# Performance work log

Measured on AMD Instinct MI355X. Metric: run time of the kernel, lower is better.

Reference implementation:

```python
import jax, jax.numpy as jnp
import numpy as np

D_MODEL = 1024
N_HEAD = 16
D_HEAD = 64
BN, T = 4, 2048


def setup_inputs() -> dict:
    key = jax.random.key(0)
    k1, k2, k3, k4 = jax.random.split(key, 4)
    x = jax.random.normal(k1, (BN, T, D_MODEL), dtype=jnp.float32)
    mask = jax.random.randint(k2, (BN, T), 0, 2, dtype=jnp.int32)
    # to_qkv: Linear(d_model, 3*d_cat, bias=False); torch weight shape [out, in]
    w_qkv = jax.random.normal(k3, (3 * N_HEAD * D_HEAD, D_MODEL), dtype=jnp.float32) / np.sqrt(D_MODEL)
    w_tail = jax.random.normal(k4, (D_MODEL, N_HEAD * D_HEAD), dtype=jnp.float32) / np.sqrt(N_HEAD * D_HEAD)
    b_tail = jnp.zeros((D_MODEL,), dtype=jnp.float32)
    return {"x": x, "mask": mask, "w_qkv": w_qkv, "w_tail": w_tail, "b_tail": b_tail}


def reference(x, mask, w_qkv, w_tail, b_tail):
    bn, t, _ = x.shape
    scale = D_HEAD ** -0.5
    # qkv: [bn, t, 3*h*d] -> view(bn,t,h,3*d) -> chunk(3) along last dim
    qkv = jnp.einsum('btm,om->bto', x, w_qkv)
    qkv = qkv.reshape(bn, t, N_HEAD, 3, D_HEAD)  # chunk layout: [q|k|v] per head
    q = qkv[..., 0, :].transpose(0, 2, 1, 3)  # [bn, h, t, d]
    k = qkv[..., 1, :].transpose(0, 2, 1, 3)
    v = qkv[..., 2, :].transpose(0, 2, 1, 3)
    dots = jnp.einsum('bhqd,bhkd->bhqk', q, k) * scale  # [bn, h, t, t]
    keep = (mask != 0)[:, None, None, :]  # [bn, 1, 1, t]
    dots = jnp.where(keep, dots, -jnp.inf)
    coef = jax.nn.softmax(dots, axis=-1)  # dropout p=0 -> identity
    attn = jnp.einsum('bhqk,bhkd->bhqd', coef, v)
    out = attn.transpose(0, 2, 1, 3).reshape(bn, t, N_HEAD * D_HEAD)
    out = jnp.einsum('btc,oc->bto', out, w_tail) + b_tail
    return out
```

## Files before the change

kernel.cpp:

```cpp
#include <hip/hip_runtime.h>
#include <hip/hip_bf16.h>
#include <stdint.h>


typedef __attribute__((ext_vector_type(8))) short short8;
typedef __attribute__((ext_vector_type(4))) short short4b;
typedef __attribute__((ext_vector_type(4))) float f32x4;

#define T_SEQ 2048
#define NHEAD 16
#define DHEAD 64
#define DMODEL 1024

#if __has_builtin(__builtin_amdgcn_exp2f)
#define EXP2(x) __builtin_amdgcn_exp2f(x)
#else
#define EXP2(x) exp2f(x)
#endif

__device__ __forceinline__ ushort f2bf(float f) {
  __bf16 h = (__bf16)f;
  unsigned short u;
  __builtin_memcpy(&u, &h, 2);
  return u;
}
__device__ __forceinline__ float bf2f(ushort b) {
  return __uint_as_float(((uint32_t)b) << 16);
}

__device__ __forceinline__ int permInv(int x) {
  return (x & 0x23) | ((x & 0x0C) << 1) | ((x & 0x10) >> 2);
}

__device__ __forceinline__ void gload_lds16(const ushort* g, ushort* l) {
  __builtin_amdgcn_global_load_lds(
      (const __attribute__((address_space(1))) void*)g,
      (__attribute__((address_space(3))) void*)l, 16, 0, 0);
}

__global__ void cvt_all(const float* __restrict__ x,
                        const float* __restrict__ wq,
                        const float* __restrict__ wt,
                        ushort* __restrict__ out,
                        int n8x, int n8q, int n8t) {
  int i = blockIdx.x * blockDim.x + threadIdx.x;
  const float* src;
  int j;
  if (i < n8x) { src = x; j = i; }
  else if (i < n8x + n8q) { src = wq; j = i - n8x; }
  else if (i < n8x + n8q + n8t) { src = wt; j = i - n8x - n8q; }
  else return;
  const float4* p = (const float4*)(src + (size_t)j * 8);
  float4 a = p[0], b = p[1];
  short8 o;
  o[0] = (short)f2bf(a.x); o[1] = (short)f2bf(a.y);
  o[2] = (short)f2bf(a.z); o[3] = (short)f2bf(a.w);
  o[4] = (short)f2bf(b.x); o[5] = (short)f2bf(b.y);
  o[6] = (short)f2bf(b.z); o[7] = (short)f2bf(b.w);
  *(short8*)(out + (size_t)i * 8) = o;
}

template <int EPI>
__launch_bounds__(256)
__global__ void gemm_bt(const ushort* __restrict__ A,
                        const ushort* __restrict__ B,
                        void* __restrict__ Cout,
                        const float* __restrict__ bias,
                        const int* __restrict__ msk,
                        int M, int N, int K) {
  __shared__ ushort sA[2][128 * 64];
  __shared__ ushort sB[2][128 * 64];
  const int tid = threadIdx.x;
  const int lane = tid & 63;
  const int wid = tid >> 6;
  const int wr = wid >> 1, wc = wid & 1;
  const int bm = blockIdx.x * 128;
  const int bn = blockIdx.y * 128;
  const int l15 = lane & 15;
  const int lg = lane >> 4;

  f32x4 acc[4][4] = {};

  auto STAGE = [&](int buf, int k0) {
#pragma unroll
    for (int r = 0; r < 4; ++r) {
      int c = r * 256 + tid;
      int row = c >> 3, ci = c & 7;
      gload_lds16(A + (size_t)(bm + row) * K + k0 + ci * 8, &sA[buf][c * 8]);
      gload_lds16(B + (size_t)(bn + row) * K + k0 + ci * 8, &sB[buf][c * 8]);
    }
  };

  STAGE(0, 0);
  __syncthreads();

  const int nk = K >> 6;
  for (int kt = 0; kt < nk; ++kt) {
    const int cur = kt & 1;
    if (kt + 1 < nk) STAGE(cur ^ 1, (kt + 1) << 6);
#pragma unroll
    for (int ks = 0; ks < 2; ++ks) {
      short8 af[4], bfr[4];
#pragma unroll
      for (int m = 0; m < 4; ++m)
        af[m] = *(const short8*)&sA[cur][(wr * 64 + m * 16 + l15) * 64 + ks * 32 + lg * 8];
#pragma unroll
      for (int n = 0; n < 4; ++n)
        bfr[n] = *(const short8*)&sB[cur][(wc * 64 + n * 16 + l15) * 64 + ks * 32 + lg * 8];
      __builtin_amdgcn_s_setprio(1);
#pragma unroll
      for (int m = 0; m < 4; ++m)
#pragma unroll
        for (int n = 0; n < 4; ++n)
          acc[m][n] = __builtin_amdgcn_mfma_f32_16x16x32_bf16(af[m], bfr[n], acc[m][n], 0, 0, 0);
      __builtin_amdgcn_s_setprio(0);
    }
    __syncthreads();
  }

  if (EPI == 0) {
    ushort* qkvb = (ushort*)Cout;
    const int b = bm >> 11;
    int mk[4][4];
#pragma unroll
    for (int m = 0; m < 4; ++m)
#pragma unroll
      for (int r = 0; r < 4; ++r) {
        int gr = bm + wr * 64 + m * 16 + lg * 4 + r;
        mk[m][r] = msk[b * T_SEQ + (gr & (T_SEQ - 1))];
      }
#pragma unroll
    for (int m = 0; m < 4; ++m)
#pragma unroll
      for (int n = 0; n < 4; ++n)
#pragma unroll
        for (int r = 0; r < 4; ++r) {
          int gr = bm + wr * 64 + m * 16 + lg * 4 + r;
          int gc = bn + wc * 64 + n * 16 + l15;
          int t = gr & (T_SEQ - 1);
          int h = gc / 192, rem = gc - h * 192;
          int sel = rem >> 6, d = rem & 63;
          size_t base = (size_t)((b * NHEAD + h) * 3 + sel) * T_SEQ * DHEAD;
          float v = acc[m][n][r];
          size_t dst;
          if (sel == 2) {
            int tp = (t & ~63) | permInv(t & 63);
            if (!mk[m][r]) v = 0.f;
            dst = base + (size_t)d * T_SEQ + tp;
          } else {
            dst = base + (size_t)t * DHEAD + d;
          }
          qkvb[dst] = f2bf(v);
        }
  } else {
    float* out = (float*)Cout;
#pragma unroll
    for (int m = 0; m < 4; ++m)
#pragma unroll
      for (int n = 0; n < 4; ++n) {
        int gc = bn + wc * 64 + n * 16 + l15;
        float bv = bias[gc];
#pragma unroll
        for (int r = 0; r < 4; ++r) {
          int gr = bm + wr * 64 + m * 16 + lg * 4 + r;
          out[(size_t)gr * N + gc] = acc[m][n][r] + bv;
        }
      }
  }
}

__launch_bounds__(256)
__global__ void attn_fwd(const ushort* __restrict__ qkv,
                         const int* __restrict__ mask,
                         ushort* __restrict__ attn) {
  __shared__ ushort sK[3][64 * 64];
  __shared__ ushort sVT[3][64 * 64];
  __shared__ ushort sInd[T_SEQ];

  const int tid = threadIdx.x;
  const int lane = tid & 63;
  const int wid = tid >> 6;
  const int l15 = lane & 15;
  const int lg = lane >> 4;
  const int bid = blockIdx.x;
  const int qt = (bid >> 3) & 15;
  const int bh = ((bid >> 7) << 3) | (bid & 7);
  const int b = bh >> 4, h = bh & 15;

  const ushort* Qp  = qkv + (size_t)(bh * 3 + 0) * T_SEQ * DHEAD;
  const ushort* Kp  = qkv + (size_t)(bh * 3 + 1) * T_SEQ * DHEAD;
  const ushort* VTp = qkv + (size_t)(bh * 3 + 2) * T_SEQ * DHEAD;
  const int* mrow = mask + b * T_SEQ;

  const int qbase = qt * 128 + wid * 32;

#pragma unroll
  for (int e = 0; e < 8; ++e) {
    int kv = tid * 8 + e;
    int p = (kv & ~63) | permInv(kv & 63);
    sInd[p] = mrow[kv] ? (ushort)0x3F80 : (ushort)0;
  }

  const float QSCALE = 0.18033688011112042f;
  short8 qf[2][2];
#pragma unroll
  for (int m = 0; m < 2; ++m)
#pragma unroll
    for (int ks = 0; ks < 2; ++ks) {
      short8 raw = *(const short8*)&Qp[(size_t)(qbase + m * 16 + l15) * 64 + ks * 32 + lg * 8];
#pragma unroll
      for (int e = 0; e < 8; ++e)
        qf[m][ks][e] = (short)f2bf(bf2f((ushort)raw[e]) * QSCALE);
    }

  f32x4 lacc[2] = {};
  f32x4 oacc[2][4] = {};

  auto STAGE = [&](int buf, int kt) {
    const int kb = kt * 64;
#pragma unroll
    for (int r2 = 0; r2 < 2; ++r2) {
      int c = r2 * 256 + tid;
      int row = c >> 3, ci = c & 7;
      int sb = (ci ^ (row & 7)) * 8;
      gload_lds16(Kp + (size_t)(kb + row) * 64 + sb, &sK[buf][c * 8]);
      gload_lds16(VTp + (size_t)row * T_SEQ + kb + sb, &sVT[buf][c * 8]);
    }
  };

  STAGE(0, 0);
  STAGE(1, 1);
  __syncthreads();

  const int NT = T_SEQ / 64;
  int cur = 0;
  for (int kt = 0; kt < NT; ++kt) {
    if (kt + 1 < NT) {
      asm volatile("s_waitcnt vmcnt(4)" ::: "memory");
    } else {
      asm volatile("s_waitcnt vmcnt(0)" ::: "memory");
    }
    __builtin_amdgcn_sched_barrier(0);
    __builtin_amdgcn_s_barrier();
    __builtin_amdgcn_sched_barrier(0);
    if (kt + 2 < NT) {
      int nb = cur + 2; if (nb >= 3) nb -= 3;
      STAGE(nb, kt + 2);
    }

    f32x4 st[4][2] = {};
#pragma unroll
    for (int ks = 0; ks < 2; ++ks) {
      short8 kf[4];
#pragma unroll
      for (int n = 0; n < 4; ++n)
        kf[n] = *(const short8*)&sK[cur][(n * 16 + l15) * 64 + ((ks * 4 + lg) ^ (l15 & 7)) * 8];
      __builtin_amdgcn_s_setprio(1);
#pragma unroll
      for (int n = 0; n < 4; ++n)
#pragma unroll
        for (int m = 0; m < 2; ++m)
          st[n][m] = __builtin_amdgcn_mfma_f32_16x16x32_bf16(kf[n], qf[m][ks], st[n][m], 0, 0, 0);
      __builtin_amdgcn_s_setprio(0);
    }

#pragma unroll
    for (int m = 0; m < 2; ++m)
#pragma unroll
      for (int n = 0; n < 4; ++n)
#pragma unroll
        for (int r = 0; r < 4; ++r)
          st[n][m][r] = EXP2(st[n][m][r]);

    short8 pa[2][2];
#pragma unroll
    for (int m = 0; m < 2; ++m)
#pragma unroll
      for (int ks = 0; ks < 2; ++ks)
#pragma unroll
        for (int e = 0; e < 4; ++e) {
          pa[m][ks][e]     = (short)f2bf(st[ks * 2][m][e]);
          pa[m][ks][4 + e] = (short)f2bf(st[ks * 2 + 1][m][e]);
        }

#pragma unroll
    for (int ks = 0; ks < 2; ++ks) {
      short8 vf[4];
#pragma unroll
      for (int dt = 0; dt < 4; ++dt)
        vf[dt] = *(const short8*)&sVT[cur][(dt * 16 + l15) * 64 + ((ks * 4 + lg) ^ (l15 & 7)) * 8];
      short8 vi = *(const short8*)&sInd[kt * 64 + ks * 32 + lg * 8];
      __builtin_amdgcn_s_setprio(1);
#pragma unroll
      for (int dt = 0; dt < 4; ++dt)
#pragma unroll
        for (int m = 0; m < 2; ++m)
          oacc[m][dt] = __builtin_amdgcn_mfma_f32_16x16x32_bf16(vf[dt], pa[m][ks], oacc[m][dt], 0, 0, 0);
#pragma unroll
      for (int m = 0; m < 2; ++m)
        lacc[m] = __builtin_amdgcn_mfma_f32_16x16x32_bf16(vi, pa[m][ks], lacc[m], 0, 0, 0);
      __builtin_amdgcn_s_setprio(0);
    }

    cur = (cur + 1 == 3) ? 0 : cur + 1;
  }

#pragma unroll
  for (int m = 0; m < 2; ++m) {
    float rl = 1.0f / lacc[m][0];
    int t = qbase + m * 16 + l15;
#pragma unroll
    for (int dt = 0; dt < 4; ++dt) {
      short4b ov;
#pragma unroll
      for (int r = 0; r < 4; ++r) ov[r] = (short)f2bf(oacc[m][dt][r] * rl);
      *(short4b*)&attn[(size_t)(b * T_SEQ + t) * DMODEL + h * DHEAD + dt * 16 + lg * 4] = ov;
    }
  }
}

extern "C" void kernel_launch(void* const* d_in, const int* in_sizes, int n_in,
                              void* d_out, int out_size, void* d_ws, size_t ws_size,
                              hipStream_t stream) {
  (void)in_sizes; (void)n_in; (void)out_size; (void)ws_size;
  const float* x      = (const float*)d_in[0];
  const int*   mask   = (const int*)d_in[1];
  const float* w_qkv  = (const float*)d_in[2];
  const float* w_tail = (const float*)d_in[3];
  const float* b_tail = (const float*)d_in[4];
  float* out = (float*)d_out;

  const size_t M = 4 * 2048;
  ushort* xb     = (ushort*)d_ws;
  ushort* wqkvb  = xb + M * DMODEL;
  ushort* wtailb = wqkvb + 3 * DMODEL * DMODEL;
  ushort* qkvb   = wtailb + DMODEL * DMODEL;
  ushort* attnb  = qkvb + (size_t)64 * 3 * T_SEQ * DHEAD;

  {
    int n8x = (int)(M * DMODEL / 8);
    int n8q = 3 * DMODEL * DMODEL / 8;
    int n8t = DMODEL * DMODEL / 8;
    int n8 = n8x + n8q + n8t;
    cvt_all<<<(n8 + 255) / 256, 256, 0, stream>>>(x, w_qkv, w_tail, xb, n8x, n8q, n8t);
  }

  gemm_bt<0><<<dim3(M / 128, 3 * DMODEL / 128), 256, 0, stream>>>(
      xb, wqkvb, qkvb, nullptr, mask, (int)M, 3 * DMODEL, DMODEL);

  attn_fwd<<<dim3(1024), 256, 0, stream>>>(qkvb, mask, attnb);

  gemm_bt<1><<<dim3(M / 128, DMODEL / 128), 256, 0, stream>>>(
      attnb, wtailb, out, b_tail, nullptr, (int)M, DMODEL, DMODEL);
}
```

Before: 218.6 us.

## Software-pipeline QK^T of next tile with exp and PV of current tile

```diff
diff --git a/kernel.cpp b/kernel.cpp
--- a/kernel.cpp
+++ b/kernel.cpp
@@ -228,82 +228,90 @@
     }
   };
 
+  auto QKT = [&](int bufi, f32x4 (*st)[2]) {
+    short8 kf0[4], kf1[4];
+#pragma unroll
+    for (int n = 0; n < 4; ++n) {
+      kf0[n] = *(const short8*)&sK[bufi][(n * 16 + l15) * 64 + (((0 + lg) ^ (l15 & 7)) * 8)];
+      kf1[n] = *(const short8*)&sK[bufi][(n * 16 + l15) * 64 + (((4 + lg) ^ (l15 & 7)) * 8)];
+    }
+    __builtin_amdgcn_s_setprio(1);
+#pragma unroll
+    for (int n = 0; n < 4; ++n)
+#pragma unroll
+      for (int m = 0; m < 2; ++m) {
+        f32x4 z = {0.f, 0.f, 0.f, 0.f};
+        st[n][m] = __builtin_amdgcn_mfma_f32_16x16x32_bf16(kf0[n], qf[m][0], z, 0, 0, 0);
+        st[n][m] = __builtin_amdgcn_mfma_f32_16x16x32_bf16(kf1[n], qf[m][1], st[n][m], 0, 0, 0);
+      }
+    __builtin_amdgcn_s_setprio(0);
+  };
+
+  const int NT = T_SEQ / 64;
+
+#define ATT_HALF(STC, STN, T, BC, BN_, BS)                                   \
+  {                                                                          \
+    _Pragma("unroll")                                                        \
+    for (int m = 0; m < 2; ++m)                                              \
+      _Pragma("unroll")                                                      \
+      for (int n = 0; n < 4; ++n)                                            \
+        _Pragma("unroll")                                                    \
+        for (int r = 0; r < 4; ++r)                                          \
+          STC[n][m][r] = EXP2(STC[n][m][r]);                                 \
+    short8 pa[2][2];                                                         \
+    _Pragma("unroll")                                                        \
+    for (int m = 0; m < 2; ++m)                                              \
+      _Pragma("unroll")                                                      \
+      for (int ks = 0; ks < 2; ++ks)                                         \
+        _Pragma("unroll")                                                    \
+        for (int e = 0; e < 4; ++e) {                                        \
+          pa[m][ks][e]     = (short)f2bf(STC[ks * 2][m][e]);                 \
+          pa[m][ks][4 + e] = (short)f2bf(STC[ks * 2 + 1][m][e]);             \
+        }                                                                    \
+    asm volatile("s_waitcnt vmcnt(0)" ::: "memory");                         \
+    __builtin_amdgcn_sched_barrier(0);                                       \
+    __builtin_amdgcn_s_barrier();                                            \
+    if ((T) + 2 < NT) STAGE(BS, (T) + 2);                                    \
+    if ((T) + 1 < NT) QKT(BN_, STN);                                         \
+    _Pragma("unroll")                                                        \
+    for (int ks = 0; ks < 2; ++ks) {                                         \
+      short8 vf[4];                                                          \
+      _Pragma("unroll")                                                      \
+      for (int dt = 0; dt < 4; ++dt)                                         \
+        vf[dt] = *(const short8*)&sVT[BC][(dt * 16 + l15) * 64 +             \
+                 (((ks * 4 + lg) ^ (l15 & 7)) * 8)];                         \
+      short8 vi = *(const short8*)&sInd[(T) * 64 + ks * 32 + lg * 8];        \
+      __builtin_amdgcn_s_setprio(1);                                         \
+      _Pragma("unroll")                                                      \
+      for (int dt = 0; dt < 4; ++dt)                                         \
+        _Pragma("unroll")                                                    \
+        for (int m = 0; m < 2; ++m)                                          \
+          oacc[m][dt] = __builtin_amdgcn_mfma_f32_16x16x32_bf16(             \
+              vf[dt], pa[m][ks], oacc[m][dt], 0, 0, 0);                      \
+      _Pragma("unroll")                                                      \
+      for (int m = 0; m < 2; ++m)                                            \
+        lacc[m] = __builtin_amdgcn_mfma_f32_16x16x32_bf16(                   \
+            vi, pa[m][ks], lacc[m], 0, 0, 0);                                \
+      __builtin_amdgcn_s_setprio(0);                                         \
+    }                                                                        \
+  }
+
   STAGE(0, 0);
   STAGE(1, 1);
   __syncthreads();
 
-  const int NT = T_SEQ / 64;
+  f32x4 stA[4][2], stB[4][2];
+  QKT(0, stA);
+
   int cur = 0;
-  for (int kt = 0; kt < NT; ++kt) {
-    if (kt + 1 < NT) {
-      asm volatile("s_waitcnt vmcnt(4)" ::: "memory");
-    } else {
-      asm volatile("s_waitcnt vmcnt(0)" ::: "memory");
-    }
-    __builtin_amdgcn_sched_barrier(0);
-    __builtin_amdgcn_s_barrier();
-    __builtin_amdgcn_sched_barrier(0);
-    if (kt + 2 < NT) {
-      int nb = cur + 2; if (nb >= 3) nb -= 3;
-      STAGE(nb, kt + 2);
-    }
-
-    f32x4 st[4][2] = {};
-#pragma unroll
-    for (int ks = 0; ks < 2; ++ks) {
-      short8 kf[4];
-#pragma unroll
-      for (int n = 0; n < 4; ++n)
-        kf[n] = *(const short8*)&sK[cur][(n * 16 + l15) * 64 + ((ks * 4 + lg) ^ (l15 & 7)) * 8];
-      __builtin_amdgcn_s_setprio(1);
-#pragma unroll
-      for (int n = 0; n < 4; ++n)
-#pragma unroll
-        for (int m = 0; m < 2; ++m)
-          st[n][m] = __builtin_amdgcn_mfma_f32_16x16x32_bf16(kf[n], qf[m][ks], st[n][m], 0, 0, 0);
-      __builtin_amdgcn_s_setprio(0);
-    }
-
-#pragma unroll
-    for (int m = 0; m < 2; ++m)
-#pragma unroll
-      for (int n = 0; n < 4; ++n)
-#pragma unroll
-        for (int r = 0; r < 4; ++r)
-          st[n][m][r] = EXP2(st[n][m][r]);
-
-    short8 pa[2][2];
-#pragma unroll
-    for (int m = 0; m < 2; ++m)
-#pragma unroll
-      for (int ks = 0; ks < 2; ++ks)
-#pragma unroll
-        for (int e = 0; e < 4; ++e) {
-          pa[m][ks][e]     = (short)f2bf(st[ks * 2][m][e]);
-          pa[m][ks][4 + e] = (short)f2bf(st[ks * 2 + 1][m][e]);
-        }
-
-#pragma unroll
-    for (int ks = 0; ks < 2; ++ks) {
-      short8 vf[4];
-#pragma unroll
-      for (int dt = 0; dt < 4; ++dt)
-        vf[dt] = *(const short8*)&sVT[cur][(dt * 16 + l15) * 64 + ((ks * 4 + lg) ^ (l15 & 7)) * 8];
-      short8 vi = *(const short8*)&sInd[kt * 64 + ks * 32 + lg * 8];
-      __builtin_amdgcn_s_setprio(1);
-#pragma unroll
-      for (int dt = 0; dt < 4; ++dt)
-#pragma unroll
-        for (int m = 0; m < 2; ++m)
-          oacc[m][dt] = __builtin_amdgcn_mfma_f32_16x16x32_bf16(vf[dt], pa[m][ks], oacc[m][dt], 0, 0, 0);
-#pragma unroll
-      for (int m = 0; m < 2; ++m)
-        lacc[m] = __builtin_amdgcn_mfma_f32_16x16x32_bf16(vi, pa[m][ks], lacc[m], 0, 0, 0);
-      __builtin_amdgcn_s_setprio(0);
-    }
-
-    cur = (cur + 1 == 3) ? 0 : cur + 1;
-  }
+  for (int kt = 0; kt < NT; kt += 2) {
+    int b1 = cur + 1; if (b1 >= 3) b1 -= 3;
+    int b2 = cur + 2; if (b2 >= 3) b2 -= 3;
+    ATT_HALF(stA, stB, kt,     cur, b1, b2);
+    ATT_HALF(stB, stA, kt + 1, b1,  b2, cur);
+    cur = b2;
+  }
+#undef ATT_HALF
 
 #pragma unroll
   for (int m = 0; m < 2; ++m) {
```

Measured after the change: 210.5 us. 3.7% less time.
